# Kernel optimization log

Measured on AMD Instinct MI355X. Metric: run time of the kernel, lower is better.

The kernel has to match this reference:

```python
import jax, jax.numpy as jnp
import numpy as np

B, S = 4, 1024           # sequences, tokens per sequence (prefill)
H, HKV, D = 32, 8, 128   # q heads, kv heads (GQA), head_dim
HID = H * D              # 4096
THETA = 10000.0


def setup_inputs() -> dict:
    key = jax.random.key(0)
    k1, k2, k3 = jax.random.split(key, 3)
    T = B * S
    hidden_states = jax.random.normal(k1, (T, HID), jnp.float32) * 0.02
    w_qkv = jax.random.normal(k2, ((H + 2 * HKV) * D, HID), jnp.float32) * 0.02
    w_dense = jax.random.normal(k3, (HID, HID), jnp.float32) * 0.02
    positions = jnp.tile(jnp.arange(S, dtype=jnp.int32), B)  # per-token position ids
    return {"positions": positions, "hidden_states": hidden_states,
            "w_qkv": w_qkv, "w_dense": w_dense}


def _rope(x, positions):
    # NeoX-style rotary embedding (vLLM rotary_dim == head_dim). x: [T, n_heads, D]
    half = D // 2
    inv_freq = 1.0 / (THETA ** (jnp.arange(half, dtype=jnp.float32) / half))
    freqs = positions.astype(jnp.float32)[:, None] * inv_freq       # [T, half]
    cos = jnp.cos(freqs)[:, None, :]
    sin = jnp.sin(freqs)[:, None, :]
    x1, x2 = x[..., :half], x[..., half:]
    return jnp.concatenate([x1 * cos - x2 * sin, x2 * cos + x1 * sin], axis=-1)


def reference(positions, hidden_states, w_qkv, w_dense):
    T = hidden_states.shape[0]
    scale = 1.0 / np.sqrt(D)
    # fused QKV projection (bias=False in config)
    qkv = hidden_states @ w_qkv.T                                   # [T, (H+2*HKV)*D]
    q, k, v = jnp.split(qkv, [H * D, (H + HKV) * D], axis=-1)
    q = q.reshape(T, H, D)
    k = k.reshape(T, HKV, D)
    v = v.reshape(T, HKV, D)
    # fused RoPE on q and k
    q = _rope(q, positions)
    k = _rope(k, positions)
    # causal GQA attention over each sequence
    G = H // HKV
    q = q.reshape(B, S, HKV, G, D)
    k = k.reshape(B, S, HKV, D)
    v = v.reshape(B, S, HKV, D)
    scores = jnp.einsum('bshgd,bthd->bhgst', q, k) * scale          # [B,HKV,G,S,S]
    causal = jnp.tril(jnp.ones((S, S), dtype=bool))
    scores = jnp.where(causal, scores, jnp.finfo(scores.dtype).min)
    probs = jax.nn.softmax(scores, axis=-1)
    attn = jnp.einsum('bhgst,bthd->bshgd', probs, v)                # [B,S,HKV,G,D]
    attn = attn.reshape(T, HID)
    # output projection (skip_bias_add, bias=False -> output only)
    return attn @ w_dense.T
```

## Files before the change

### kernel.cpp

```cpp
#include <hip/hip_runtime.h>

typedef short bf16x8 __attribute__((ext_vector_type(8)));
typedef float f32x4 __attribute__((ext_vector_type(4)));
typedef float f32x16 __attribute__((ext_vector_type(16)));

__device__ __forceinline__ ushort f2bf(float f) {
  union { float f; unsigned u; } x; x.f = f;
  unsigned r = x.u + 0x7fffu + ((x.u >> 16) & 1u);
  return (ushort)(r >> 16);
}
__device__ __forceinline__ float bf2f(ushort u) {
  union { unsigned u; float f; } x; x.u = ((unsigned)u) << 16; return x.f;
}
__device__ __forceinline__ void load_lds16(const void* g, void* l) {
  __builtin_amdgcn_global_load_lds((const __attribute__((address_space(1))) void*)g,
                                   (__attribute__((address_space(3))) void*)l, 16, 0, 0);
}
__device__ __forceinline__ void store_out(float* p, float v) { *p = v; }
__device__ __forceinline__ void store_out(ushort* p, float v) { *p = f2bf(v); }

__global__ __launch_bounds__(256) void cast_kernel(const float* __restrict__ in,
                                                   ushort* __restrict__ out, int n4) {
  int i = blockIdx.x * 256 + threadIdx.x;
  if (i < n4) {
    float4 v = ((const float4*)in)[i];
    ushort4 o;
    o.x = f2bf(v.x); o.y = f2bf(v.y); o.z = f2bf(v.z); o.w = f2bf(v.w);
    ((ushort4*)out)[i] = o;
  }
}

template <typename OutT>
__global__ __launch_bounds__(256) void gemm_bt(const ushort* __restrict__ A,
                                               const ushort* __restrict__ B,
                                               OutT* __restrict__ C,
                                               int M, int N, int K) {
  __shared__ ushort As[128 * 64];
  __shared__ ushort Bs[128 * 64];
  const int tid = threadIdx.x;
  const int wave = tid >> 6, lane = tid & 63;
  const int half = lane >> 5, l32 = lane & 31;
  const int m0 = blockIdx.y * 128, n0 = blockIdx.x * 128;
  const int wr = wave >> 1, wc = wave & 1;
  const int sgrow = lane >> 3;
  const int sgchunk = ((lane & 7) ^ sgrow) * 8;

  f32x16 acc[2][2] = {};

  for (int k0 = 0; k0 < K; k0 += 64) {
    __syncthreads();
#pragma unroll
    for (int i = 0; i < 4; ++i) {
      const int rg = wave * 32 + i * 8;
      load_lds16(A + (size_t)(m0 + rg + sgrow) * K + k0 + sgchunk, As + rg * 64);
      load_lds16(B + (size_t)(n0 + rg + sgrow) * K + k0 + sgchunk, Bs + rg * 64);
    }
    __syncthreads();
#pragma unroll
    for (int s = 0; s < 4; ++s) {
      bf16x8 af[2], bfr[2];
#pragma unroll
      for (int i = 0; i < 2; ++i) {
        const int row = wr * 64 + i * 32 + l32;
        af[i] = *(const bf16x8*)(As + row * 64 + (((s * 2 + half) ^ (row & 7)) * 8));
      }
#pragma unroll
      for (int j = 0; j < 2; ++j) {
        const int row = wc * 64 + j * 32 + l32;
        bfr[j] = *(const bf16x8*)(Bs + row * 64 + (((s * 2 + half) ^ (row & 7)) * 8));
      }
#pragma unroll
      for (int i = 0; i < 2; ++i)
#pragma unroll
        for (int j = 0; j < 2; ++j)
          acc[i][j] = __builtin_amdgcn_mfma_f32_32x32x16_bf16(af[i], bfr[j], acc[i][j], 0, 0, 0);
    }
  }
#pragma unroll
  for (int i = 0; i < 2; ++i)
#pragma unroll
    for (int j = 0; j < 2; ++j)
#pragma unroll
      for (int r = 0; r < 16; ++r) {
        const int row = m0 + wr * 64 + i * 32 + (r & 3) + 8 * (r >> 2) + 4 * half;
        const int col = n0 + wc * 64 + j * 32 + l32;
        store_out(C + (size_t)row * N + col, acc[i][j][r]);
      }
}

__global__ __launch_bounds__(256) void rope_kernel(const int* __restrict__ pos,
                                                   ushort* __restrict__ qkv) {
  const int rid = blockIdx.x * 4 + (threadIdx.x >> 6);
  const int d = threadIdx.x & 63;
  const int t = rid / 40;
  const int hh = rid - t * 40;
  ushort* p = qkv + (size_t)t * 6144 + (hh < 32 ? hh * 128 : 4096 + (hh - 32) * 128);
  const float inv_freq = powf(10000.0f, -(float)d * (1.0f / 64.0f));
  const float fr = (float)pos[t] * inv_freq;
  float sn, cs;
  sincosf(fr, &sn, &cs);
  const float x1 = bf2f(p[d]);
  const float x2 = bf2f(p[d + 64]);
  p[d] = f2bf(x1 * cs - x2 * sn);
  p[d + 64] = f2bf(x2 * cs + x1 * sn);
}

__global__ __launch_bounds__(256) void attn_fused(const ushort* __restrict__ qkv,
                                                  ushort* __restrict__ outb) {
  const int bid = blockIdx.x;
  const int pair = bid & 7;
  const int h = (bid >> 3) & 31;
  const int b = bid >> 8;
  const int kvh = h >> 2;
  const int tid = threadIdx.x, wave = tid >> 6, lane = tid & 63;
  const int quad = lane >> 4, lx = lane & 15;

  __shared__ ushort Ks[64 * 128];
  __shared__ ushort Vt[128 * 64];
  __shared__ ushort Ps[64 * 64];

  const size_t tb = (size_t)b * 1024;
  const float scale = 0.08838834764831843f;

#pragma unroll
  for (int phase = 0; phase < 2; ++phase) {
    const int qt64 = phase ? (15 - pair) : pair;
    const int qrow0 = qt64 * 64 + wave * 16;

    bf16x8 qf[4];
#pragma unroll
    for (int ks = 0; ks < 4; ++ks)
      qf[ks] = *(const bf16x8*)(qkv + (tb + qrow0 + lx) * 6144 + h * 128 + ks * 32 + quad * 8);

    f32x4 o[8] = {};
    float mst[4], lst[4];
#pragma unroll
    for (int r = 0; r < 4; ++r) { mst[r] = -1e30f; lst[r] = 0.f; }

    const int nkt = qt64 + 1;
    for (int it = 0; it < nkt; ++it) {
      const int kb = it * 64;
      __syncthreads();
#pragma unroll
      for (int i = 0; i < 4; ++i) {
        const int rg = wave * 16 + i * 4;
        const int row = rg + quad;
        load_lds16(qkv + (tb + kb + row) * 6144 + 4096 + kvh * 128 + ((lx ^ (row & 7)) * 8),
                   Ks + rg * 128);
      }
      {
        const ushort* vp = qkv + (tb + kb + lane) * 6144 + 5120 + kvh * 128 + wave * 32;
#pragma unroll
        for (int c = 0; c < 4; ++c) {
          bf16x8 v8 = *(const bf16x8*)(vp + c * 8);
#pragma unroll
          for (int e = 0; e < 8; ++e) {
            const int d = wave * 32 + c * 8 + e;
            Vt[d * 64 + (((lane >> 3) ^ (d & 7)) * 8) + (lane & 7)] = (ushort)v8[e];
          }
        }
      }
      __syncthreads();

      f32x4 s[4] = {};
#pragma unroll
      for (int ks = 0; ks < 4; ++ks) {
        bf16x8 kf[4];
#pragma unroll
        for (int kt = 0; kt < 4; ++kt)
          kf[kt] = *(const bf16x8*)(Ks + (kt * 16 + lx) * 128 + (((ks * 4 + quad) ^ (lx & 7)) * 8));
#pragma unroll
        for (int kt = 0; kt < 4; ++kt)
          s[kt] = __builtin_amdgcn_mfma_f32_16x16x32_bf16(qf[ks], kf[kt], s[kt], 0, 0, 0);
      }

      const bool diag = (kb + 63 > qrow0);
#pragma unroll
      for (int r = 0; r < 4; ++r) {
        const int row = qrow0 + quad * 4 + r;
        float mx = -1e30f;
#pragma unroll
        for (int kt = 0; kt < 4; ++kt) {
          float sv = s[kt][r] * scale;
          if (diag && (kb + kt * 16 + lx > row)) sv = -1e30f;
          s[kt][r] = sv;
          mx = fmaxf(mx, sv);
        }
        mx = fmaxf(mx, __shfl_xor(mx, 1));
        mx = fmaxf(mx, __shfl_xor(mx, 2));
        mx = fmaxf(mx, __shfl_xor(mx, 4));
        mx = fmaxf(mx, __shfl_xor(mx, 8));
        const float mnew = fmaxf(mst[r], mx);
        const float alpha = __expf(mst[r] - mnew);
        mst[r] = mnew;
        float rs = 0.f;
#pragma unroll
        for (int kt = 0; kt < 4; ++kt) {
          const float pv = __expf(s[kt][r] - mnew);
          s[kt][r] = pv;
          rs += pv;
        }
        rs += __shfl_xor(rs, 1); rs += __shfl_xor(rs, 2);
        rs += __shfl_xor(rs, 4); rs += __shfl_xor(rs, 8);
        lst[r] = lst[r] * alpha + rs;
#pragma unroll
        for (int dt = 0; dt < 8; ++dt) o[dt][r] *= alpha;
        const int prow = wave * 16 + quad * 4 + r;
#pragma unroll
        for (int kt = 0; kt < 4; ++kt)
          Ps[prow * 64 + (((kt * 2 + (lx >> 3)) ^ (prow & 7)) * 8) + (lx & 7)] = f2bf(s[kt][r]);
      }
      __syncthreads();

#pragma unroll
      for (int ks2 = 0; ks2 < 2; ++ks2) {
        const int prow = wave * 16 + lx;
        bf16x8 pf = *(const bf16x8*)(Ps + prow * 64 + (((ks2 * 4 + quad) ^ (lx & 7)) * 8));
#pragma unroll
        for (int dt = 0; dt < 8; ++dt) {
          bf16x8 vf = *(const bf16x8*)(Vt + (dt * 16 + lx) * 64 + (((ks2 * 4 + quad) ^ (lx & 7)) * 8));
          o[dt] = __builtin_amdgcn_mfma_f32_16x16x32_bf16(pf, vf, o[dt], 0, 0, 0);
        }
      }
    }

#pragma unroll
    for (int r = 0; r < 4; ++r) {
      const float inv = 1.f / lst[r];
      const int row = qrow0 + quad * 4 + r;
#pragma unroll
      for (int dt = 0; dt < 8; ++dt)
        outb[(tb + row) * 4096 + h * 128 + dt * 16 + lx] = f2bf(o[dt][r] * inv);
    }
  }
}

extern "C" void kernel_launch(void* const* d_in, const int* in_sizes, int n_in,
                              void* d_out, int out_size, void* d_ws, size_t ws_size,
                              hipStream_t stream) {
  const int* positions = (const int*)d_in[0];
  const float* hidden  = (const float*)d_in[1];
  const float* w_qkv   = (const float*)d_in[2];
  const float* w_dense = (const float*)d_in[3];
  float* out = (float*)d_out;

  ushort* hidden_bf = (ushort*)d_ws;
  ushort* wqkv_bf   = hidden_bf + (size_t)16777216;
  ushort* wdense_bf = wqkv_bf   + (size_t)25165824;
  ushort* qkv_bf    = wdense_bf + (size_t)16777216;
  ushort* attn_bf   = qkv_bf    + (size_t)25165824;

  cast_kernel<<<16384, 256, 0, stream>>>(hidden,  hidden_bf, 4194304);
  cast_kernel<<<24576, 256, 0, stream>>>(w_qkv,   wqkv_bf,   6291456);
  cast_kernel<<<16384, 256, 0, stream>>>(w_dense, wdense_bf, 4194304);

  gemm_bt<ushort><<<dim3(48, 32), 256, 0, stream>>>(hidden_bf, wqkv_bf, qkv_bf, 4096, 6144, 4096);

  rope_kernel<<<40960, 256, 0, stream>>>(positions, qkv_bf);

  attn_fused<<<1024, 256, 0, stream>>>(qkv_bf, attn_bf);

  gemm_bt<float><<<dim3(32, 32), 256, 0, stream>>>(attn_bf, wdense_bf, out, 4096, 4096, 4096);
}
```

Before: 790.2 us.

## Replace GEMM with 256x256 tile, double-buffered LDS pipeline and 16x16 MFMA

Replaces the 128x128 single-buffered bf16 GEMM with a 512-thread kernel that computes a 256x256 output tile. It double-buffers the LDS tiles and interleaves async global->LDS loads for the next K-steps with MFMA quadrants, using explicit barriers, waitcnt and setprio. It also switches from 32x32x16 to 16x16x32 MFMA. The aim is to hide global load latency and raise arithmetic intensity per block, at the cost of 128KB LDS per block (occupancy of one block per CU), a heavy register load (128 accumulator floats per lane), and only 384 or 256 blocks per GEMM.

```diff
diff --git a/kernel.cpp b/kernel.cpp
--- a/kernel.cpp
+++ b/kernel.cpp
@@ -2,7 +2,6 @@
 
 typedef short bf16x8 __attribute__((ext_vector_type(8)));
 typedef float f32x4 __attribute__((ext_vector_type(4)));
-typedef float f32x16 __attribute__((ext_vector_type(16)));
 
 __device__ __forceinline__ ushort f2bf(float f) {
   union { float f; unsigned u; } x; x.f = f;
@@ -30,62 +29,104 @@
   }
 }
 
+#define PBAR() do { asm volatile("" ::: "memory"); __builtin_amdgcn_s_barrier(); \
+                    asm volatile("" ::: "memory"); } while (0)
+#define WAITL() do { asm volatile("s_waitcnt lgkmcnt(0)" ::: "memory"); \
+                     __builtin_amdgcn_sched_barrier(0); } while (0)
+
 template <typename OutT>
-__global__ __launch_bounds__(256) void gemm_bt(const ushort* __restrict__ A,
+__global__ __launch_bounds__(512) void gemm256(const ushort* __restrict__ A,
                                                const ushort* __restrict__ B,
                                                OutT* __restrict__ C,
                                                int M, int N, int K) {
-  __shared__ ushort As[128 * 64];
-  __shared__ ushort Bs[128 * 64];
+  __shared__ ushort As[2][256 * 64];
+  __shared__ ushort Bs[2][256 * 64];
   const int tid = threadIdx.x;
   const int wave = tid >> 6, lane = tid & 63;
-  const int half = lane >> 5, l32 = lane & 31;
-  const int m0 = blockIdx.y * 128, n0 = blockIdx.x * 128;
-  const int wr = wave >> 1, wc = wave & 1;
+  const int quad = lane >> 4, lx = lane & 15;
+  const int wr = wave >> 2, wc = wave & 3;
+  const int m0 = blockIdx.y * 256, n0 = blockIdx.x * 256;
+  const int NT = K >> 6;
   const int sgrow = lane >> 3;
   const int sgchunk = ((lane & 7) ^ sgrow) * 8;
 
-  f32x16 acc[2][2] = {};
-
-  for (int k0 = 0; k0 < K; k0 += 64) {
-    __syncthreads();
-#pragma unroll
-    for (int i = 0; i < 4; ++i) {
-      const int rg = wave * 32 + i * 8;
-      load_lds16(A + (size_t)(m0 + rg + sgrow) * K + k0 + sgchunk, As + rg * 64);
-      load_lds16(B + (size_t)(n0 + rg + sgrow) * K + k0 + sgchunk, Bs + rg * 64);
-    }
-    __syncthreads();
-#pragma unroll
-    for (int s = 0; s < 4; ++s) {
-      bf16x8 af[2], bfr[2];
-#pragma unroll
-      for (int i = 0; i < 2; ++i) {
-        const int row = wr * 64 + i * 32 + l32;
-        af[i] = *(const bf16x8*)(As + row * 64 + (((s * 2 + half) ^ (row & 7)) * 8));
-      }
-#pragma unroll
-      for (int j = 0; j < 2; ++j) {
-        const int row = wc * 64 + j * 32 + l32;
-        bfr[j] = *(const bf16x8*)(Bs + row * 64 + (((s * 2 + half) ^ (row & 7)) * 8));
-      }
-#pragma unroll
-      for (int i = 0; i < 2; ++i)
-#pragma unroll
-        for (int j = 0; j < 2; ++j)
-          acc[i][j] = __builtin_amdgcn_mfma_f32_32x32x16_bf16(af[i], bfr[j], acc[i][j], 0, 0, 0);
-    }
+  f32x4 acc[8][4] = {};
+  bf16x8 af[4][2], bfr[4][2];
+
+#define STAGE_A(T, H)                                                         \
+  do {                                                                        \
+    _Pragma("unroll") for (int i_ = 0; i_ < 2; ++i_) {                        \
+      const int rg_ = (H) * 128 + wave * 16 + i_ * 8;                         \
+      load_lds16(A + (size_t)(m0 + rg_ + sgrow) * K + (T) * 64 + sgchunk,     \
+                 &As[(T) & 1][rg_ * 64]);                                     \
+    }                                                                         \
+  } while (0)
+#define STAGE_B(T, H)                                                         \
+  do {                                                                        \
+    _Pragma("unroll") for (int i_ = 0; i_ < 2; ++i_) {                        \
+      const int rg_ = (H) * 128 + wave * 16 + i_ * 8;                         \
+      load_lds16(B + (size_t)(n0 + rg_ + sgrow) * K + (T) * 64 + sgchunk,     \
+                 &Bs[(T) & 1][rg_ * 64]);                                     \
+    }                                                                         \
+  } while (0)
+#define READ_A(QM)                                                            \
+  _Pragma("unroll") for (int mm = 0; mm < 4; ++mm)                            \
+  _Pragma("unroll") for (int s = 0; s < 2; ++s)                               \
+    af[mm][s] = *(const bf16x8*)(curA + (wr * 128 + ((QM) * 4 + mm) * 16 + lx) * 64 \
+                                 + (((s * 4 + quad) ^ (lx & 7)) * 8));
+#define READ_B(NLO)                                                           \
+  _Pragma("unroll") for (int nn = 0; nn < 2; ++nn)                            \
+  _Pragma("unroll") for (int s = 0; s < 2; ++s)                               \
+    bfr[(NLO) + nn][s] = *(const bf16x8*)(curB + (wc * 64 + ((NLO) + nn) * 16 + lx) * 64 \
+                                 + (((s * 4 + quad) ^ (lx & 7)) * 8));
+#define MFMA_Q(QM, QN)                                                        \
+  __builtin_amdgcn_s_setprio(1);                                              \
+  _Pragma("unroll") for (int mm = 0; mm < 4; ++mm)                            \
+  _Pragma("unroll") for (int nn = 0; nn < 2; ++nn)                            \
+  _Pragma("unroll") for (int s = 0; s < 2; ++s)                               \
+    acc[(QM) * 4 + mm][(QN) * 2 + nn] = __builtin_amdgcn_mfma_f32_16x16x32_bf16( \
+        af[mm][s], bfr[(QN) * 2 + nn][s], acc[(QM) * 4 + mm][(QN) * 2 + nn], 0, 0, 0); \
+  __builtin_amdgcn_s_setprio(0);
+
+  STAGE_A(0, 0); STAGE_A(0, 1); STAGE_B(0, 0); STAGE_B(0, 1);
+  if (NT > 1) { STAGE_B(1, 0); STAGE_B(1, 1); }
+
+  for (int t = 0; t < NT; ++t) {
+    asm volatile("" ::: "memory");
+    if (t == NT - 1) { asm volatile("s_waitcnt vmcnt(0)" ::: "memory"); }
+    else             { asm volatile("s_waitcnt vmcnt(4)" ::: "memory"); }
+    __builtin_amdgcn_s_barrier();
+    asm volatile("" ::: "memory");
+    const ushort* curA = As[t & 1];
+    const ushort* curB = Bs[t & 1];
+    READ_A(0); READ_B(0);
+    if (t + 1 < NT) STAGE_A(t + 1, 0);
+    PBAR(); WAITL(); MFMA_Q(0, 0); PBAR();
+    READ_B(2);
+    if (t + 1 < NT) STAGE_A(t + 1, 1);
+    PBAR(); WAITL(); MFMA_Q(0, 1); PBAR();
+    READ_A(1);
+    if (t + 2 < NT) STAGE_B(t + 2, 0);
+    PBAR(); WAITL(); MFMA_Q(1, 0); PBAR();
+    if (t + 2 < NT) STAGE_B(t + 2, 1);
+    PBAR(); MFMA_Q(1, 1); PBAR();
   }
-#pragma unroll
-  for (int i = 0; i < 2; ++i)
-#pragma unroll
-    for (int j = 0; j < 2; ++j)
-#pragma unroll
-      for (int r = 0; r < 16; ++r) {
-        const int row = m0 + wr * 64 + i * 32 + (r & 3) + 8 * (r >> 2) + 4 * half;
-        const int col = n0 + wc * 64 + j * 32 + l32;
-        store_out(C + (size_t)row * N + col, acc[i][j][r]);
-      }
+
+#pragma unroll
+  for (int m = 0; m < 8; ++m)
+#pragma unroll
+    for (int n = 0; n < 4; ++n)
+#pragma unroll
+      for (int r = 0; r < 4; ++r) {
+        const int row = m0 + wr * 128 + m * 16 + quad * 4 + r;
+        const int col = n0 + wc * 64 + n * 16 + lx;
+        store_out(C + (size_t)row * N + col, acc[m][n][r]);
+      }
+#undef STAGE_A
+#undef STAGE_B
+#undef READ_A
+#undef READ_B
+#undef MFMA_Q
 }
 
 __global__ __launch_bounds__(256) void rope_kernel(const int* __restrict__ pos,
@@ -254,11 +295,11 @@
   cast_kernel<<<24576, 256, 0, stream>>>(w_qkv,   wqkv_bf,   6291456);
   cast_kernel<<<16384, 256, 0, stream>>>(w_dense, wdense_bf, 4194304);
 
-  gemm_bt<ushort><<<dim3(48, 32), 256, 0, stream>>>(hidden_bf, wqkv_bf, qkv_bf, 4096, 6144, 4096);
+  gemm256<ushort><<<dim3(24, 16), 512, 0, stream>>>(hidden_bf, wqkv_bf, qkv_bf, 4096, 6144, 4096);
 
   rope_kernel<<<40960, 256, 0, stream>>>(positions, qkv_bf);
 
   attn_fused<<<1024, 256, 0, stream>>>(qkv_bf, attn_bf);
 
-  gemm_bt<float><<<dim3(32, 32), 256, 0, stream>>>(attn_bf, wdense_bf, out, 4096, 4096, 4096);
-}
+  gemm256<float><<<dim3(16, 16), 512, 0, stream>>>(attn_bf, wdense_bf, out, 4096, 4096, 4096);
+}
```

Measured after the change: 782.2 us. No clear change (-1.0%).
